# Optimization experiments

Measured on AMD Instinct MI355X. Metric: run time of the kernel, lower is better.

Reference implementation:

```python
import jax, jax.numpy as jnp
import numpy as np

C = 256          # in_channels
CQK = C // 8     # query/key channels


def setup_inputs() -> dict:
    key = jax.random.key(0)
    ks = jax.random.split(key, 10)
    B, H, W = 4, 64, 64
    x1 = jax.random.normal(ks[0], (B, C, H, W), dtype=jnp.float32)
    x2 = jax.random.normal(ks[1], (B, C, H, W), dtype=jnp.float32)
    s = 0.05
    Wq = jax.random.normal(ks[2], (CQK, C), dtype=jnp.float32) * s
    bq = jax.random.normal(ks[3], (CQK,), dtype=jnp.float32) * s
    Wk = jax.random.normal(ks[4], (CQK, C), dtype=jnp.float32) * s
    bk = jax.random.normal(ks[5], (CQK,), dtype=jnp.float32) * s
    Wv = jax.random.normal(ks[6], (C, C), dtype=jnp.float32) * s
    bv = jax.random.normal(ks[7], (C,), dtype=jnp.float32) * s
    Wc = jax.random.normal(ks[8], (C, 2 * C), dtype=jnp.float32) * s
    bc = jax.random.normal(ks[9], (C,), dtype=jnp.float32) * s
    return {"x1": x1, "x2": x2, "Wq": Wq, "bq": bq, "Wk": Wk, "bk": bk,
            "Wv": Wv, "bv": bv, "Wc": Wc, "bc": bc}


def _proj(x_flat, Wm, b):
    # 1x1 conv == channel GEMM: [B,C,N] -> [B,Cout,N]
    return jnp.einsum('oc,bcn->bon', Wm, x_flat) + b[None, :, None]


def reference(x1, x2, Wq, bq, Wk, bk, Wv, bv, Wc, bc):
    B, Cin, H, W = x1.shape
    N = H * W
    xf1 = x1.reshape(B, Cin, N)
    xf2 = x2.reshape(B, Cin, N)
    q1 = _proj(xf1, Wq, bq)   # [B,CQK,N]
    k1 = _proj(xf1, Wk, bk)
    v1 = _proj(xf1, Wv, bv)   # [B,C,N]
    q2 = _proj(xf2, Wq, bq)
    k2 = _proj(xf2, Wk, bk)
    v2 = _proj(xf2, Wv, bv)

    def branch(q, k, v_other):
        # attn[b,i,j] = softmax_j(q[:, :, i] . k[:, :, j])
        attn = jax.nn.softmax(jnp.einsum('bci,bcj->bij', q, k), axis=2)
        # attended[b,c,i] = sum_j v_other[b,c,j] * attn[b,i,j]
        return jnp.einsum('bcj,bij->bci', v_other, attn)

    att1 = branch(q1, k1, v2).reshape(B, Cin, H, W)
    att2 = branch(q2, k2, v1).reshape(B, Cin, H, W)

    def combine(a, b_att):
        cat = jnp.concatenate((a, b_att), axis=1).reshape(B, 2 * Cin, N)
        comb = (jnp.einsum('oc,bcn->bon', Wc, cat) + bc[None, :, None]).reshape(B, Cin, H, W)
        return jnp.abs(comb).sum(axis=1, keepdims=True)

    # NOTE: original code uses x1 in BOTH combines (faithful to source)
    out1 = combine(x1, att1)
    out2 = combine(x1, att2)
    return out1, out2
```

## Files before the change

### kernel.cpp

```cpp
#include <hip/hip_runtime.h>
#include <cstdint>

#define LOG2E 1.4426950408889634f

typedef __bf16 bf16x8 __attribute__((ext_vector_type(8)));
typedef float f32x4 __attribute__((ext_vector_type(4)));

#define MFMA16(a,b,c) __builtin_amdgcn_mfma_f32_16x16x32_bf16((a),(b),(c),0,0,0)
#define EXP2(x) __builtin_amdgcn_exp2f(x)

#define LDS_BARRIER() asm volatile("s_waitcnt lgkmcnt(0)\n\ts_barrier" ::: "memory")

constexpr size_t OFF_XT = 0;
constexpr size_t OFF_QT = 8388608;
constexpr size_t OFF_KT = 9437184;
constexpr size_t OFF_V  = 10485760;
constexpr size_t OFF_WQ = 18874368;
constexpr size_t OFF_WK = 18882560;
constexpr size_t OFF_WV = 18890752;
constexpr size_t OFF_WC = 18956288;

static __device__ __forceinline__ unsigned short f2b(float a) {
  return __builtin_bit_cast(unsigned short, (__bf16)a);
}
static __device__ __forceinline__ unsigned pk2(float a, float b) {
  return ((unsigned)f2b(b) << 16) | (unsigned)f2b(a);
}

__global__ __launch_bounds__(256) void prep_kernel(
    const float* __restrict__ x1, const float* __restrict__ x2,
    const float* __restrict__ Wq, const float* __restrict__ Wk,
    const float* __restrict__ Wv, const float* __restrict__ Wc,
    short* __restrict__ ws)
{
  __shared__ float tile[64][65];
  const int tid = threadIdx.x;
  const int blk = blockIdx.x;
  if (blk < 2048) {
    const int nt = blk & 63, ct = (blk >> 6) & 3, b = (blk >> 8) & 3, inp = blk >> 10;
    const float* x = (inp ? x2 : x1) + (size_t)(b * 256 + ct * 64) * 4096 + nt * 64;
#pragma unroll
    for (int p = 0; p < 4; ++p) {
      int r = p * 16 + (tid >> 4);
      float4 v = *(const float4*)(x + (size_t)r * 4096 + (tid & 15) * 4);
      tile[r][(tid & 15) * 4 + 0] = v.x;
      tile[r][(tid & 15) * 4 + 1] = v.y;
      tile[r][(tid & 15) * 4 + 2] = v.z;
      tile[r][(tid & 15) * 4 + 3] = v.w;
    }
    __syncthreads();
    const int n = tid >> 2, c0 = (tid & 3) * 16;
    unsigned u[8];
#pragma unroll
    for (int k = 0; k < 8; ++k)
      u[k] = pk2(tile[c0 + 2 * k][n], tile[c0 + 2 * k + 1][n]);
    short* dst = ws + OFF_XT + (size_t)((inp * 4 + b) * 4096 + nt * 64 + n) * 256 + ct * 64 + c0;
    uint4 s0; s0.x = u[0]; s0.y = u[1]; s0.z = u[2]; s0.w = u[3];
    uint4 s1; s1.x = u[4]; s1.y = u[5]; s1.z = u[6]; s1.w = u[7];
    *(uint4*)(dst) = s0;
    *(uint4*)(dst + 8) = s1;
  } else {
    int idx = (blk - 2048) * 4096 + tid * 16;
    const float* src; short* dst; int off;
    if (idx < 8192)        { src = Wq; dst = ws + OFF_WQ; off = idx; }
    else if (idx < 16384)  { src = Wk; dst = ws + OFF_WK; off = idx - 8192; }
    else if (idx < 81920)  { src = Wv; dst = ws + OFF_WV; off = idx - 16384; }
    else                   { src = Wc; dst = ws + OFF_WC; off = idx - 81920; }
#pragma unroll
    for (int j = 0; j < 16; ++j) dst[off + j] = (short)f2b(src[off + j]);
  }
}

static __device__ __forceinline__ void proj_qk_body(
    short* __restrict__ ws, const float* __restrict__ bq, const float* __restrict__ bk,
    int blk, int tid)
{
  const int lane = tid & 63, wid = tid >> 6;
  const int g = lane >> 4, l15 = lane & 15;
  const int nt = blk & 31, b = (blk >> 5) & 3, inp = blk >> 7;
  const int n0 = nt * 128 + wid * 32;

  const short* xp  = ws + OFF_XT + (size_t)(inp * 4 + b) * (4096 * 256) + (size_t)n0 * 256;
  const short* wqp = ws + OFF_WQ;
  const short* wkp = ws + OFF_WK;
  short* Qt = ws + OFF_QT + (size_t)(inp * 4 + b) * (4096 * 32);
  short* Kt = ws + OFF_KT + (size_t)(inp * 4 + b) * (4096 * 32);

  const f32x4 z4 = {0.f, 0.f, 0.f, 0.f};
  f32x4 aq[2][2], ak[2][2];
#pragma unroll
  for (int i = 0; i < 2; ++i)
#pragma unroll
    for (int j = 0; j < 2; ++j) { aq[i][j] = z4; ak[i][j] = z4; }

#pragma unroll
  for (int ks = 0; ks < 8; ++ks) {
    bf16x8 xa[2];
#pragma unroll
    for (int ns = 0; ns < 2; ++ns)
      xa[ns] = *(const bf16x8*)(xp + (size_t)(ns * 16 + l15) * 256 + ks * 32 + g * 8);
#pragma unroll
    for (int os = 0; os < 2; ++os) {
      bf16x8 wq8 = *(const bf16x8*)(wqp + (size_t)(os * 16 + l15) * 256 + ks * 32 + g * 8);
      bf16x8 wk8 = *(const bf16x8*)(wkp + (size_t)(os * 16 + l15) * 256 + ks * 32 + g * 8);
#pragma unroll
      for (int ns = 0; ns < 2; ++ns) {
        aq[ns][os] = MFMA16(xa[ns], wq8, aq[ns][os]);
        ak[ns][os] = MFMA16(xa[ns], wk8, ak[ns][os]);
      }
    }
  }
  float bqv[2], bkv[2];
#pragma unroll
  for (int os = 0; os < 2; ++os) { bqv[os] = bq[os * 16 + l15]; bkv[os] = bk[os * 16 + l15]; }
#pragma unroll
  for (int ns = 0; ns < 2; ++ns)
#pragma unroll
    for (int os = 0; os < 2; ++os)
#pragma unroll
      for (int r = 0; r < 4; ++r) {
        int n = n0 + ns * 16 + g * 4 + r;
        int o = os * 16 + l15;
        Qt[(size_t)n * 32 + o] = (short)f2b((aq[ns][os][r] + bqv[os]) * LOG2E);
        Kt[(size_t)n * 32 + o] = (short)f2b(ak[ns][os][r] + bkv[os]);
      }
}

static __device__ __forceinline__ void proj_v_body(
    short* __restrict__ ws, const float* __restrict__ bv, char* vl, int blk, int tid)
{
  const int lane = tid & 63, wid = tid >> 6;
  const int g = lane >> 4, l15 = lane & 15;
  const int nt = blk & 63, b = (blk >> 6) & 3, inp = blk >> 8;
  const int n0 = nt * 64;

  const short* xp  = ws + OFF_XT + (size_t)(inp * 4 + b) * (4096 * 256) + (size_t)n0 * 256;
  const short* wvp = ws + OFF_WV;
  short* Vp = ws + OFF_V + (size_t)(inp * 4 + b) * (256 * 4096);

  const f32x4 z4 = {0.f, 0.f, 0.f, 0.f};
  f32x4 acc[4][4];
#pragma unroll
  for (int i = 0; i < 4; ++i)
#pragma unroll
    for (int j = 0; j < 4; ++j) acc[i][j] = z4;

#pragma unroll
  for (int ks = 0; ks < 8; ++ks) {
    bf16x8 xa[4];
#pragma unroll
    for (int ns = 0; ns < 4; ++ns)
      xa[ns] = *(const bf16x8*)(xp + (size_t)(ns * 16 + l15) * 256 + ks * 32 + g * 8);
#pragma unroll
    for (int os = 0; os < 4; ++os) {
      bf16x8 wv8 = *(const bf16x8*)(wvp + (size_t)(wid * 64 + os * 16 + l15) * 256 + ks * 32 + g * 8);
#pragma unroll
      for (int ns = 0; ns < 4; ++ns)
        acc[os][ns] = MFMA16(wv8, xa[ns], acc[os][ns]);
    }
  }
  float bvv[4][4];
#pragma unroll
  for (int os = 0; os < 4; ++os)
#pragma unroll
    for (int r = 0; r < 4; ++r) bvv[os][r] = bv[wid * 64 + os * 16 + g * 4 + r];

  char* myl = vl + wid * 8192;
#pragma unroll
  for (int os = 0; os < 4; ++os)
#pragma unroll
    for (int ns = 0; ns < 4; ++ns)
#pragma unroll
      for (int r = 0; r < 4; ++r) {
        int o_loc = os * 16 + g * 4 + r;
        int n_loc = ns * 16 + l15;
        *(short*)(myl + o_loc * 128 + ((n_loc * 2) ^ ((o_loc & 7) << 4))) =
            (short)f2b(acc[os][ns][r] + bvv[os][r]);
      }
#pragma unroll
  for (int sc = 0; sc < 4; ++sc)
#pragma unroll
    for (int sj = 0; sj < 2; ++sj) {
      int c_loc = sc * 16 + l15;
      bf16x8 row = *(const bf16x8*)(myl + c_loc * 128 +
                                    (((unsigned)(sj * 64 + g * 16)) ^ ((c_loc & 7) << 4)));
      size_t c16 = (size_t)(wid * 4 + sc);
      size_t j32 = (size_t)(nt * 2 + sj);
      *(bf16x8*)(Vp + (c16 * 128 + j32) * 512 + lane * 8) = row;
    }
}

__global__ __launch_bounds__(256) void proj_kernel(
    short* __restrict__ ws, const float* __restrict__ bq,
    const float* __restrict__ bk, const float* __restrict__ bv)
{
  __shared__ __align__(16) char vl[32768];
  const int tid = threadIdx.x, blk = blockIdx.x;
  if (blk < 256) proj_qk_body(ws, bq, bk, blk, tid);
  else           proj_v_body(ws, bv, vl, blk - 256, tid);
}

__global__ __launch_bounds__(256, 2) void attn_kernel(
    short* __restrict__ ws, const float* __restrict__ bc, float* __restrict__ out)
{
  const int tid = threadIdx.x, lane = tid & 63, wid = tid >> 6;
  const int g = lane >> 4, l15 = lane & 15;
  const int bid = ((blockIdx.x & 7) << 6) | (blockIdx.x >> 3);
  const int itile = bid & 63, b = (bid >> 6) & 3, br = bid >> 8;
  const int i0 = itile * 64;

  __shared__ __align__(16) char sm[34048];
  float* l_l  = (float*)(sm + 32768);
  float* part = (float*)(sm + 33024);

  const short* Qb  = ws + OFF_QT + (size_t)(br * 4 + b) * (4096 * 32);
  const short* Kb  = ws + OFF_KT + (size_t)(br * 4 + b) * (4096 * 32);
  const short* Vb  = ws + OFF_V  + (size_t)((1 - br) * 4 + b) * (256 * 4096);
  const short* xb  = ws + OFF_XT + (size_t)b * (4096 * 256);
  const short* Wcb = ws + OFF_WC;

  const f32x4 z4 = {0.f, 0.f, 0.f, 0.f};
  const int irow = wid * 16 + l15;
  const unsigned sw = (unsigned)((irow & 7) << 4);

  bf16x8 qf = *(const bf16x8*)(Qb + (size_t)(i0 + wid * 16 + l15) * 32 + g * 8);

  f32x4 oc[4][4];
#pragma unroll
  for (int i = 0; i < 4; ++i)
#pragma unroll
    for (int j = 0; j < 4; ++j) oc[i][j] = z4;
  float l_run = 0.f;

#pragma unroll
  for (int tt = 0; tt < 2; ++tt) {
    bf16x8 kt[4];
#pragma unroll
    for (int jt = 0; jt < 4; ++jt)
      kt[jt] = *(const bf16x8*)(Kb + (size_t)(tt * 64 + jt * 16 + l15) * 32 + g * 8);
    f32x4 s0[4];
#pragma unroll
    for (int jt = 0; jt < 4; ++jt) s0[jt] = MFMA16(kt[jt], qf, z4);
    char* Pw = sm + tt * 8192;
#pragma unroll
    for (int jt = 0; jt < 4; ++jt) {
#pragma unroll
      for (int r = 0; r < 4; ++r) {
        float p = EXP2(s0[jt][r]);
        s0[jt][r] = p;
        l_run += p;
      }
      unsigned long long u =
          ((unsigned long long)pk2(s0[jt][2], s0[jt][3]) << 32) | pk2(s0[jt][0], s0[jt][1]);
      *(unsigned long long*)(Pw + irow * 128 + (((unsigned)(jt * 32 + g * 8)) ^ sw)) = u;
    }
  }

  bf16x8 kf[4], va[2][4], pb[2][2][4];
#pragma unroll
  for (int jt = 0; jt < 4; ++jt)
    kf[jt] = *(const bf16x8*)(Kb + (size_t)(128 + jt * 16 + l15) * 32 + g * 8);
#pragma unroll
  for (int ks = 0; ks < 2; ++ks)
#pragma unroll
    for (int cs = 0; cs < 4; ++cs)
      va[ks][cs] = *(const bf16x8*)(Vb + ((size_t)(wid * 4 + cs) * 128 + ks) * 512 + lane * 8);

  LDS_BARRIER();

#pragma unroll
  for (int ks = 0; ks < 2; ++ks)
#pragma unroll
    for (int it = 0; it < 4; ++it) {
      int i = it * 16 + l15;
      pb[0][ks][it] = *(const bf16x8*)(sm + i * 128 +
                                       (((unsigned)(ks * 64 + g * 16)) ^ ((i & 7) << 4)));
    }
  LDS_BARRIER();

#define ATTN_BODY(TC, CUR, NXT, DO_S, PREFK, PREFV, DO_PB)                               \
  do {                                                                                   \
    if (DO_PB) {                                                                         \
      const char* Pr = sm + (((TC) + 1) & 1) * 8192;                                     \
      _Pragma("unroll")                                                                  \
      for (int ks = 0; ks < 2; ++ks)                                                     \
        _Pragma("unroll")                                                                \
        for (int it = 0; it < 4; ++it) {                                                 \
          int i = it * 16 + l15;                                                         \
          pb[NXT][ks][it] = *(const bf16x8*)(Pr + i * 128 +                              \
                                (((unsigned)(ks * 64 + g * 16)) ^ ((i & 7) << 4)));      \
        }                                                                                \
    }                                                                                    \
    f32x4 st[4];                                                                         \
    if (DO_S) {                                                                          \
      _Pragma("unroll")                                                                  \
      for (int jt = 0; jt < 4; ++jt) st[jt] = MFMA16(kf[jt], qf, z4);                    \
    }                                                                                    \
    if (PREFK) {                                                                         \
      _Pragma("unroll")                                                                  \
      for (int jt = 0; jt < 4; ++jt)                                                     \
        kf[jt] = *(const bf16x8*)(Kb + (size_t)(((TC) + 3) * 64 + jt * 16 + l15) * 32 + g * 8); \
    }                                                                                    \
    __builtin_amdgcn_s_setprio(1);                                                       \
    _Pragma("unroll")                                                                    \
    for (int ks = 0; ks < 2; ++ks)                                                       \
      _Pragma("unroll")                                                                  \
      for (int it = 0; it < 4; ++it)                                                     \
        _Pragma("unroll")                                                                \
        for (int cs = 0; cs < 4; ++cs)                                                   \
          oc[cs][it] = MFMA16(va[ks][cs], pb[CUR][ks][it], oc[cs][it]);                  \
    __builtin_amdgcn_s_setprio(0);                                                       \
    if (PREFV) {                                                                         \
      _Pragma("unroll")                                                                  \
      for (int ks = 0; ks < 2; ++ks)                                                     \
        _Pragma("unroll")                                                                \
        for (int cs = 0; cs < 4; ++cs)                                                   \
          va[ks][cs] = *(const bf16x8*)(Vb + ((size_t)(wid * 4 + cs) * 128 +             \
                                              (size_t)((TC) + 1) * 2 + ks) * 512 + lane * 8); \
    }                                                                                    \
    if (DO_S) {                                                                          \
      char* Pw = sm + ((TC) & 1) * 8192;                                                 \
      _Pragma("unroll")                                                                  \
      for (int jt = 0; jt < 4; ++jt) {                                                   \
        _Pragma("unroll")                                                                \
        for (int r = 0; r < 4; ++r) {                                                    \
          float p = EXP2(st[jt][r]);                                                     \
          st[jt][r] = p;                                                                 \
          l_run += p;                                                                    \
        }                                                                                \
        unsigned long long u =                                                           \
            ((unsigned long long)pk2(st[jt][2], st[jt][3]) << 32) | pk2(st[jt][0], st[jt][1]); \
        *(unsigned long long*)(Pw + irow * 128 + (((unsigned)(jt * 32 + g * 8)) ^ sw)) = u; \
      }                                                                                  \
    }                                                                                    \
    LDS_BARRIER();                                                                       \
  } while (0)

  for (int t = 0; t < 60; t += 2) {
    ATTN_BODY(t,     0, 1, 1, 1, 1, 1);
    ATTN_BODY(t + 1, 1, 0, 1, 1, 1, 1);
  }
  ATTN_BODY(60, 0, 1, 1, 1, 1, 1);
  ATTN_BODY(61, 1, 0, 1, 0, 1, 1);
  ATTN_BODY(62, 0, 1, 0, 0, 1, 1);
  ATTN_BODY(63, 1, 0, 0, 0, 0, 0);
#undef ATTN_BODY

  l_run += __shfl_xor(l_run, 16);
  l_run += __shfl_xor(l_run, 32);

  if (g == 0) l_l[irow] = l_run;
  __syncthreads();
  float rl[4];
#pragma unroll
  for (int it = 0; it < 4; ++it) rl[it] = 1.f / l_l[it * 16 + l15];

#pragma unroll
  for (int cs = 0; cs < 4; ++cs)
#pragma unroll
    for (int it = 0; it < 4; ++it) {
      f32x4 v = oc[cs][it];
      v *= rl[it];
      int i = it * 16 + l15;
      unsigned byte = (unsigned)(i * 512) +
                      (((unsigned)((wid * 64 + cs * 16 + g * 4) * 2)) ^ ((i & 7) << 4));
      unsigned long long u = ((unsigned long long)pk2(v[2], v[3]) << 32) | pk2(v[0], v[1]);
      *(unsigned long long*)(sm + byte) = u;
    }
  __syncthreads();

  f32x4 cc[4][4];
#pragma unroll
  for (int i = 0; i < 4; ++i)
#pragma unroll
    for (int j = 0; j < 4; ++j) cc[i][j] = z4;

#pragma unroll
  for (int ks = 0; ks < 16; ++ks) {
    bf16x8 bfr[4];
#pragma unroll
    for (int ns = 0; ns < 4; ++ns) {
      int n = ns * 16 + l15;
      if (ks < 8)
        bfr[ns] = *(const bf16x8*)(xb + (size_t)(i0 + n) * 256 + ks * 32 + g * 8);
      else
        bfr[ns] = *(const bf16x8*)(sm + n * 512 +
                                   (((unsigned)((ks - 8) * 64 + g * 16)) ^ ((n & 7) << 4)));
    }
#pragma unroll
    for (int os = 0; os < 4; ++os) {
      bf16x8 af = *(const bf16x8*)(Wcb + (size_t)(wid * 64 + os * 16 + l15) * 512 + ks * 32 + g * 8);
#pragma unroll
      for (int ns = 0; ns < 4; ++ns)
        cc[os][ns] = MFMA16(af, bfr[ns], cc[os][ns]);
    }
  }
  float bcv[4][4];
#pragma unroll
  for (int os = 0; os < 4; ++os)
#pragma unroll
    for (int r = 0; r < 4; ++r) bcv[os][r] = bc[wid * 64 + os * 16 + g * 4 + r];

#pragma unroll
  for (int ns = 0; ns < 4; ++ns) {
    float tsum = 0.f;
#pragma unroll
    for (int os = 0; os < 4; ++os)
#pragma unroll
      for (int r = 0; r < 4; ++r)
        tsum += fabsf(cc[os][ns][r] + bcv[os][r]);
    tsum += __shfl_xor(tsum, 16);
    tsum += __shfl_xor(tsum, 32);
    if (g == 0) part[wid * 64 + ns * 16 + l15] = tsum;
  }
  __syncthreads();
  if (tid < 64) {
    float s = part[tid] + part[64 + tid] + part[128 + tid] + part[192 + tid];
    out[(size_t)br * 16384 + b * 4096 + i0 + tid] = s;
  }
}

extern "C" void kernel_launch(void* const* d_in, const int* in_sizes, int n_in,
                              void* d_out, int out_size, void* d_ws, size_t ws_size,
                              hipStream_t stream) {
  const float* x1 = (const float*)d_in[0];
  const float* x2 = (const float*)d_in[1];
  const float* Wq = (const float*)d_in[2];
  const float* bq = (const float*)d_in[3];
  const float* Wk = (const float*)d_in[4];
  const float* bk = (const float*)d_in[5];
  const float* Wv = (const float*)d_in[6];
  const float* bv = (const float*)d_in[7];
  const float* Wc = (const float*)d_in[8];
  const float* bc = (const float*)d_in[9];
  short* ws = (short*)d_ws;
  float* out = (float*)d_out;

  prep_kernel<<<2100, 256, 0, stream>>>(x1, x2, Wq, Wk, Wv, Wc, ws);
  proj_kernel<<<768, 256, 0, stream>>>(ws, bq, bk, bv);
  attn_kernel<<<512, 256, 0, stream>>>(ws, bc, out);
}
```

Baseline: 135.3 us.

## Fuse input transpose/convert into projection kernel via LDS-staged bf16 tile

The fp32-to-bf16 transpose of x is moved into the projection kernel, which now stages each 64-pixel by 256-channel bf16 tile in swizzled LDS. The Q/K and V projections then read their operands from LDS instead of re-reading the transposed global buffer, and the weight conversion becomes its own small kernel. This cuts a global round trip of the activations and one dependency between kernels, but each block now does a serial 4-step load/transpose loop with barriers and uses more LDS, which may lower occupancy. The transposed x is still written to global memory, presumably because the attention kernel reads it for the combine step.

```diff
diff --git a/kernel.cpp b/kernel.cpp
--- a/kernel.cpp
+++ b/kernel.cpp
@@ -27,177 +27,158 @@
   return ((unsigned)f2b(b) << 16) | (unsigned)f2b(a);
 }
 
-__global__ __launch_bounds__(256) void prep_kernel(
-    const float* __restrict__ x1, const float* __restrict__ x2,
+__global__ __launch_bounds__(256) void weights_kernel(
     const float* __restrict__ Wq, const float* __restrict__ Wk,
     const float* __restrict__ Wv, const float* __restrict__ Wc,
     short* __restrict__ ws)
 {
-  __shared__ float tile[64][65];
-  const int tid = threadIdx.x;
+  int idx = blockIdx.x * 4096 + threadIdx.x * 16;
+  const float* src; short* dst; int off;
+  if (idx < 8192)        { src = Wq; dst = ws + OFF_WQ; off = idx; }
+  else if (idx < 16384)  { src = Wk; dst = ws + OFF_WK; off = idx - 8192; }
+  else if (idx < 81920)  { src = Wv; dst = ws + OFF_WV; off = idx - 16384; }
+  else                   { src = Wc; dst = ws + OFF_WC; off = idx - 81920; }
+#pragma unroll
+  for (int j = 0; j < 16; ++j) dst[off + j] = (short)f2b(src[off + j]);
+}
+
+__global__ __launch_bounds__(256) void proj_fused_kernel(
+    const float* __restrict__ x1, const float* __restrict__ x2,
+    short* __restrict__ ws, const float* __restrict__ bq,
+    const float* __restrict__ bk, const float* __restrict__ bv)
+{
+  __shared__ __align__(16) char smem[49408];
+  float (*tile)[65] = (float(*)[65])smem;
+  char* xbt = smem + 16640;
+
+  const int tid = threadIdx.x, lane = tid & 63, wid = tid >> 6;
+  const int g = lane >> 4, l15 = lane & 15;
   const int blk = blockIdx.x;
-  if (blk < 2048) {
-    const int nt = blk & 63, ct = (blk >> 6) & 3, b = (blk >> 8) & 3, inp = blk >> 10;
-    const float* x = (inp ? x2 : x1) + (size_t)(b * 256 + ct * 64) * 4096 + nt * 64;
+  const int nt = blk & 63, b = (blk >> 6) & 3, inp = blk >> 8;
+  const int n0 = nt * 64;
+
+  const float* xsrc = (inp ? x2 : x1) + (size_t)b * 256 * 4096;
+
+  const int pn = tid >> 2, pc0 = (tid & 3) * 16;
+  const unsigned swn = (unsigned)((pn & 7) << 4);
+#pragma unroll
+  for (int ct = 0; ct < 4; ++ct) {
 #pragma unroll
     for (int p = 0; p < 4; ++p) {
       int r = p * 16 + (tid >> 4);
-      float4 v = *(const float4*)(x + (size_t)r * 4096 + (tid & 15) * 4);
+      float4 v = *(const float4*)(xsrc + (size_t)(ct * 64 + r) * 4096 + n0 + (tid & 15) * 4);
       tile[r][(tid & 15) * 4 + 0] = v.x;
       tile[r][(tid & 15) * 4 + 1] = v.y;
       tile[r][(tid & 15) * 4 + 2] = v.z;
       tile[r][(tid & 15) * 4 + 3] = v.w;
     }
     __syncthreads();
-    const int n = tid >> 2, c0 = (tid & 3) * 16;
     unsigned u[8];
 #pragma unroll
     for (int k = 0; k < 8; ++k)
-      u[k] = pk2(tile[c0 + 2 * k][n], tile[c0 + 2 * k + 1][n]);
-    short* dst = ws + OFF_XT + (size_t)((inp * 4 + b) * 4096 + nt * 64 + n) * 256 + ct * 64 + c0;
+      u[k] = pk2(tile[pc0 + 2 * k][pn], tile[pc0 + 2 * k + 1][pn]);
     uint4 s0; s0.x = u[0]; s0.y = u[1]; s0.z = u[2]; s0.w = u[3];
     uint4 s1; s1.x = u[4]; s1.y = u[5]; s1.z = u[6]; s1.w = u[7];
+    short* dst = ws + OFF_XT + (size_t)((inp * 4 + b) * 4096 + n0 + pn) * 256 + ct * 64 + pc0;
     *(uint4*)(dst) = s0;
     *(uint4*)(dst + 8) = s1;
-  } else {
-    int idx = (blk - 2048) * 4096 + tid * 16;
-    const float* src; short* dst; int off;
-    if (idx < 8192)        { src = Wq; dst = ws + OFF_WQ; off = idx; }
-    else if (idx < 16384)  { src = Wk; dst = ws + OFF_WK; off = idx - 8192; }
-    else if (idx < 81920)  { src = Wv; dst = ws + OFF_WV; off = idx - 16384; }
-    else                   { src = Wc; dst = ws + OFF_WC; off = idx - 81920; }
-#pragma unroll
-    for (int j = 0; j < 16; ++j) dst[off + j] = (short)f2b(src[off + j]);
-  }
-}
-
-static __device__ __forceinline__ void proj_qk_body(
-    short* __restrict__ ws, const float* __restrict__ bq, const float* __restrict__ bk,
-    int blk, int tid)
-{
-  const int lane = tid & 63, wid = tid >> 6;
-  const int g = lane >> 4, l15 = lane & 15;
-  const int nt = blk & 31, b = (blk >> 5) & 3, inp = blk >> 7;
-  const int n0 = nt * 128 + wid * 32;
-
-  const short* xp  = ws + OFF_XT + (size_t)(inp * 4 + b) * (4096 * 256) + (size_t)n0 * 256;
-  const short* wqp = ws + OFF_WQ;
-  const short* wkp = ws + OFF_WK;
-  short* Qt = ws + OFF_QT + (size_t)(inp * 4 + b) * (4096 * 32);
-  short* Kt = ws + OFF_KT + (size_t)(inp * 4 + b) * (4096 * 32);
+    char* row = xbt + pn * 512;
+    *(uint4*)(row + (((unsigned)(ct * 128 + pc0 * 2)) ^ swn)) = s0;
+    *(uint4*)(row + (((unsigned)(ct * 128 + pc0 * 2 + 16)) ^ swn)) = s1;
+    __syncthreads();
+  }
 
   const f32x4 z4 = {0.f, 0.f, 0.f, 0.f};
-  f32x4 aq[2][2], ak[2][2];
-#pragma unroll
-  for (int i = 0; i < 2; ++i)
-#pragma unroll
-    for (int j = 0; j < 2; ++j) { aq[i][j] = z4; ak[i][j] = z4; }
-
-#pragma unroll
-  for (int ks = 0; ks < 8; ++ks) {
-    bf16x8 xa[2];
-#pragma unroll
-    for (int ns = 0; ns < 2; ++ns)
-      xa[ns] = *(const bf16x8*)(xp + (size_t)(ns * 16 + l15) * 256 + ks * 32 + g * 8);
+#define LDX(ROW, KS) (*(const bf16x8*)(xbt + (ROW) * 512 + \
+    (((unsigned)((KS) * 64 + g * 16)) ^ ((unsigned)(((ROW) & 7) << 4)))))
+
+  {
+    const short* wqp = ws + OFF_WQ;
+    const short* wkp = ws + OFF_WK;
+    short* Qt = ws + OFF_QT + (size_t)(inp * 4 + b) * (4096 * 32);
+    short* Kt = ws + OFF_KT + (size_t)(inp * 4 + b) * (4096 * 32);
+    f32x4 aq[2], ak[2];
+#pragma unroll
+    for (int os = 0; os < 2; ++os) { aq[os] = z4; ak[os] = z4; }
+    const int nrow = wid * 16 + l15;
+#pragma unroll
+    for (int ks = 0; ks < 8; ++ks) {
+      bf16x8 xa = LDX(nrow, ks);
+#pragma unroll
+      for (int os = 0; os < 2; ++os) {
+        bf16x8 wq8 = *(const bf16x8*)(wqp + (size_t)(os * 16 + l15) * 256 + ks * 32 + g * 8);
+        bf16x8 wk8 = *(const bf16x8*)(wkp + (size_t)(os * 16 + l15) * 256 + ks * 32 + g * 8);
+        aq[os] = MFMA16(xa, wq8, aq[os]);
+        ak[os] = MFMA16(xa, wk8, ak[os]);
+      }
+    }
 #pragma unroll
     for (int os = 0; os < 2; ++os) {
-      bf16x8 wq8 = *(const bf16x8*)(wqp + (size_t)(os * 16 + l15) * 256 + ks * 32 + g * 8);
-      bf16x8 wk8 = *(const bf16x8*)(wkp + (size_t)(os * 16 + l15) * 256 + ks * 32 + g * 8);
-#pragma unroll
-      for (int ns = 0; ns < 2; ++ns) {
-        aq[ns][os] = MFMA16(xa[ns], wq8, aq[ns][os]);
-        ak[ns][os] = MFMA16(xa[ns], wk8, ak[ns][os]);
+      float bqv = bq[os * 16 + l15], bkv = bk[os * 16 + l15];
+#pragma unroll
+      for (int r = 0; r < 4; ++r) {
+        int n = n0 + wid * 16 + g * 4 + r;
+        int o = os * 16 + l15;
+        Qt[(size_t)n * 32 + o] = (short)f2b((aq[os][r] + bqv) * LOG2E);
+        Kt[(size_t)n * 32 + o] = (short)f2b(ak[os][r] + bkv);
       }
     }
   }
-  float bqv[2], bkv[2];
-#pragma unroll
-  for (int os = 0; os < 2; ++os) { bqv[os] = bq[os * 16 + l15]; bkv[os] = bk[os * 16 + l15]; }
-#pragma unroll
-  for (int ns = 0; ns < 2; ++ns)
-#pragma unroll
-    for (int os = 0; os < 2; ++os)
-#pragma unroll
-      for (int r = 0; r < 4; ++r) {
-        int n = n0 + ns * 16 + g * 4 + r;
-        int o = os * 16 + l15;
-        Qt[(size_t)n * 32 + o] = (short)f2b((aq[ns][os][r] + bqv[os]) * LOG2E);
-        Kt[(size_t)n * 32 + o] = (short)f2b(ak[ns][os][r] + bkv[os]);
+
+  {
+    const short* wvp = ws + OFF_WV;
+    short* Vp = ws + OFF_V + (size_t)(inp * 4 + b) * (256 * 4096);
+    f32x4 acc[4][4];
+#pragma unroll
+    for (int i = 0; i < 4; ++i)
+#pragma unroll
+      for (int j = 0; j < 4; ++j) acc[i][j] = z4;
+
+#pragma unroll
+    for (int ks = 0; ks < 8; ++ks) {
+      bf16x8 xa[4];
+#pragma unroll
+      for (int ns = 0; ns < 4; ++ns) xa[ns] = LDX(ns * 16 + l15, ks);
+#pragma unroll
+      for (int os = 0; os < 4; ++os) {
+        bf16x8 wv8 = *(const bf16x8*)(wvp + (size_t)(wid * 64 + os * 16 + l15) * 256 + ks * 32 + g * 8);
+#pragma unroll
+        for (int ns = 0; ns < 4; ++ns)
+          acc[os][ns] = MFMA16(wv8, xa[ns], acc[os][ns]);
       }
-}
-
-static __device__ __forceinline__ void proj_v_body(
-    short* __restrict__ ws, const float* __restrict__ bv, char* vl, int blk, int tid)
-{
-  const int lane = tid & 63, wid = tid >> 6;
-  const int g = lane >> 4, l15 = lane & 15;
-  const int nt = blk & 63, b = (blk >> 6) & 3, inp = blk >> 8;
-  const int n0 = nt * 64;
-
-  const short* xp  = ws + OFF_XT + (size_t)(inp * 4 + b) * (4096 * 256) + (size_t)n0 * 256;
-  const short* wvp = ws + OFF_WV;
-  short* Vp = ws + OFF_V + (size_t)(inp * 4 + b) * (256 * 4096);
-
-  const f32x4 z4 = {0.f, 0.f, 0.f, 0.f};
-  f32x4 acc[4][4];
-#pragma unroll
-  for (int i = 0; i < 4; ++i)
-#pragma unroll
-    for (int j = 0; j < 4; ++j) acc[i][j] = z4;
-
-#pragma unroll
-  for (int ks = 0; ks < 8; ++ks) {
-    bf16x8 xa[4];
-#pragma unroll
-    for (int ns = 0; ns < 4; ++ns)
-      xa[ns] = *(const bf16x8*)(xp + (size_t)(ns * 16 + l15) * 256 + ks * 32 + g * 8);
-#pragma unroll
-    for (int os = 0; os < 4; ++os) {
-      bf16x8 wv8 = *(const bf16x8*)(wvp + (size_t)(wid * 64 + os * 16 + l15) * 256 + ks * 32 + g * 8);
+    }
+    float bvv[4][4];
+#pragma unroll
+    for (int os = 0; os < 4; ++os)
+#pragma unroll
+      for (int r = 0; r < 4; ++r) bvv[os][r] = bv[wid * 64 + os * 16 + g * 4 + r];
+
+    __syncthreads();
+    char* myl = xbt + wid * 8192;
+#pragma unroll
+    for (int os = 0; os < 4; ++os)
 #pragma unroll
       for (int ns = 0; ns < 4; ++ns)
-        acc[os][ns] = MFMA16(wv8, xa[ns], acc[os][ns]);
-    }
-  }
-  float bvv[4][4];
-#pragma unroll
-  for (int os = 0; os < 4; ++os)
-#pragma unroll
-    for (int r = 0; r < 4; ++r) bvv[os][r] = bv[wid * 64 + os * 16 + g * 4 + r];
-
-  char* myl = vl + wid * 8192;
-#pragma unroll
-  for (int os = 0; os < 4; ++os)
-#pragma unroll
-    for (int ns = 0; ns < 4; ++ns)
-#pragma unroll
-      for (int r = 0; r < 4; ++r) {
-        int o_loc = os * 16 + g * 4 + r;
-        int n_loc = ns * 16 + l15;
-        *(short*)(myl + o_loc * 128 + ((n_loc * 2) ^ ((o_loc & 7) << 4))) =
-            (short)f2b(acc[os][ns][r] + bvv[os][r]);
+#pragma unroll
+        for (int r = 0; r < 4; ++r) {
+          int o_loc = os * 16 + g * 4 + r;
+          int n_loc = ns * 16 + l15;
+          *(short*)(myl + o_loc * 128 + ((n_loc * 2) ^ ((o_loc & 7) << 4))) =
+              (short)f2b(acc[os][ns][r] + bvv[os][r]);
+        }
+#pragma unroll
+    for (int sc = 0; sc < 4; ++sc)
+#pragma unroll
+      for (int sj = 0; sj < 2; ++sj) {
+        int c_loc = sc * 16 + l15;
+        bf16x8 row = *(const bf16x8*)(myl + c_loc * 128 +
+                                      (((unsigned)(sj * 64 + g * 16)) ^ ((c_loc & 7) << 4)));
+        size_t c16 = (size_t)(wid * 4 + sc);
+        size_t j32 = (size_t)(nt * 2 + sj);
+        *(bf16x8*)(Vp + (c16 * 128 + j32) * 512 + lane * 8) = row;
       }
-#pragma unroll
-  for (int sc = 0; sc < 4; ++sc)
-#pragma unroll
-    for (int sj = 0; sj < 2; ++sj) {
-      int c_loc = sc * 16 + l15;
-      bf16x8 row = *(const bf16x8*)(myl + c_loc * 128 +
-                                    (((unsigned)(sj * 64 + g * 16)) ^ ((c_loc & 7) << 4)));
-      size_t c16 = (size_t)(wid * 4 + sc);
-      size_t j32 = (size_t)(nt * 2 + sj);
-      *(bf16x8*)(Vp + (c16 * 128 + j32) * 512 + lane * 8) = row;
-    }
-}
-
-__global__ __launch_bounds__(256) void proj_kernel(
-    short* __restrict__ ws, const float* __restrict__ bq,
-    const float* __restrict__ bk, const float* __restrict__ bv)
-{
-  __shared__ __align__(16) char vl[32768];
-  const int tid = threadIdx.x, blk = blockIdx.x;
-  if (blk < 256) proj_qk_body(ws, bq, bk, blk, tid);
-  else           proj_v_body(ws, bv, vl, blk - 256, tid);
+  }
+#undef LDX
 }
 
 __global__ __launch_bounds__(256, 2) void attn_kernel(
@@ -436,7 +417,7 @@
   short* ws = (short*)d_ws;
   float* out = (float*)d_out;
 
-  prep_kernel<<<2100, 256, 0, stream>>>(x1, x2, Wq, Wk, Wv, Wc, ws);
-  proj_kernel<<<768, 256, 0, stream>>>(ws, bq, bk, bv);
+  weights_kernel<<<52, 256, 0, stream>>>(Wq, Wk, Wv, Wc, ws);
+  proj_fused_kernel<<<512, 256, 0, stream>>>(x1, x2, ws, bq, bk, bv);
   attn_kernel<<<512, 256, 0, stream>>>(ws, bc, out);
 }
```

Result: faster. 130.1 us (-3.8%).
